# Optimization experiments

Measured on AMD Instinct MI355X. Metric: run time of the kernel, lower is better.

The kernel has to match this reference:

```python
import jax, jax.numpy as jnp
import numpy as np

N = 4_000_000   # total points, 4 per frame
E = N // 4      # edges per subset (idx % 4 == 1, 2, 3)
SQRT2 = float(np.sqrt(2.0))
SQRT3 = float(np.sqrt(3.0))


def _smear(d, num, start=0.0, stop=5.0):
    # GaussianSmearing: exp(-0.5/dx^2 * (d - mu_k)^2), mu_k = linspace(start, stop, num)
    offsets = jnp.linspace(start, stop, num, dtype=d.dtype)
    coeff = -0.5 / (offsets[1] - offsets[0]) ** 2
    return jnp.exp(coeff * (d[:, None] - offsets[None, :]) ** 2)


def setup_inputs() -> dict:
    key = jax.random.key(0)
    ks = jax.random.split(key, 12)
    w = lambda k, s: jax.random.normal(k, s, jnp.float32) * 0.1
    return {
        "ligand_pos": jax.random.normal(ks[0], (N, 3), jnp.float32),
        "receptor_pos": jax.random.normal(ks[1], (N, 3), jnp.float32),
        "W1_sso": w(ks[2], (5, 4, 20)),   # 0e x 0e -> 0e
        "W1_svv": w(ks[3], (5, 5)),       # 0e x 1e -> 1e
        "W1_vsv": w(ks[4], (4, 5)),       # 1e x 0e -> 1e
        "W1_vvo": w(ks[5], (20,)),        # 1e x 1e -> 0e
        "W1_vvv": w(ks[6], (5,)),         # 1e x 1e -> 1e
        "W2_sso": w(ks[7], (20, 5, 9)),
        "W2_svv": w(ks[8], (20,)),
        "W2_vsv": w(ks[9], (5, 5)),
        "W2_vvo": w(ks[10], (5, 9)),
        "W2_vvv": w(ks[11], (5,)),
    }


def reference(ligand_pos, receptor_pos, W1_sso, W1_svv, W1_vsv, W1_vvo, W1_vvv,
              W2_sso, W2_svv, W2_vsv, W2_vvo, W2_vvv):
    edge_vec = ligand_pos - receptor_pos                      # [N,3]
    dist = jnp.sqrt(jnp.sum(edge_vec * edge_vec, -1) + 1e-12)  # [N]
    unit = edge_vec / dist[:, None]

    emb5 = _smear(dist, 5)  # scalars for '5x0e' inputs (features 1, 3)
    emb4 = _smear(dist, 4)  # scalars for '4x0e' input (features 2)

    # edge subsets idx % 4 == 1, 2, 3 (strided gathers)
    s1, v1 = emb5[1::4], unit[1::4]   # [E,5], [E,3]
    s2, v2 = emb4[2::4], unit[2::4]   # [E,4], [E,3]
    s3, v3 = emb5[3::4], unit[3::4]   # [E,5], [E,3]

    # ---- tp1: (5x0e + 1e) x (4x0e + 1e) -> 20x0e + 5x1e ----
    dot12 = jnp.sum(v1 * v2, -1) / SQRT3        # CG 1e x 1e -> 0e
    cross12 = jnp.cross(v1, v2) / SQRT2         # CG 1e x 1e -> 1e
    out_s = (jnp.einsum('ei,ej,ijk->ek', s1, s2, W1_sso)
             + dot12[:, None] * W1_vvo[None, :]) / np.sqrt(21.0)   # fan_in 5*4+1
    out_v = (jnp.einsum('ei,ec,ik->ekc', s1, v2, W1_svv)
             + jnp.einsum('ec,ej,jk->ekc', v1, s2, W1_vsv)
             + cross12[:, None, :] * W1_vvv[None, :, None]) / np.sqrt(10.0)  # fan_in 5+4+1

    # ---- tp2: (20x0e + 5x1e) x (5x0e + 1e) -> 9x0e + 1x1e ----
    dot2 = jnp.einsum('ekc,ec->ek', out_v, v3) / SQRT3          # [E,5]
    cross2 = jnp.cross(out_v, v3[:, None, :]) / SQRT2           # [E,5,3]
    o_s = (jnp.einsum('ei,ej,ijk->ek', out_s, s3, W2_sso)
           + jnp.einsum('ek,ko->eo', dot2, W2_vvo)) / np.sqrt(105.0)  # fan_in 100+5
    o_v = (jnp.einsum('ei,ec,i->ec', out_s, v3, W2_svv)
           + jnp.einsum('ekc,ej,kj->ec', out_v, s3, W2_vsv)
           + jnp.einsum('ekc,k->ec', cross2, W2_vvv)) / np.sqrt(50.0)  # fan_in 20+25+5

    out = jnp.concatenate([o_s, o_v], -1)  # [E,12]
    s_rot, s_tr = out[:, 0:3], out[:, 3:6]
    t_rot, t_tr = out[:, 6:9], out[:, 9:12]
    return jnp.stack([s_rot, s_tr, t_rot, t_tr], 0)  # [4,E,3]
```

## Files before the change

kernel.cpp:

```cpp
#include <hip/hip_runtime.h>
#include <math.h>


#define WS_W12  0
#define WS_WV   900
#define WS_WS   945
#define WS_CS   965
#define WS_SVV  966
#define WS_VSV  991
#define WS_VVV1 1011
#define WS_VSV2 1016
#define WS_VVV2 1041
#define WS_VVO2 1046
#define WS_TOT  1091

__global__ __launch_bounds__(256) void fds_precompose(
    const float* __restrict__ W1_sso, const float* __restrict__ W1_svv,
    const float* __restrict__ W1_vsv, const float* __restrict__ W1_vvo,
    const float* __restrict__ W1_vvv, const float* __restrict__ W2_sso,
    const float* __restrict__ W2_svv, const float* __restrict__ W2_vsv,
    const float* __restrict__ W2_vvo, const float* __restrict__ W2_vvv,
    float* __restrict__ ws)
{
    const float I2 = 0.70710678118654752f, I3 = 0.57735026918962576f;
    const float I10 = 0.31622776601683794f, I21 = 0.21821789023599239f;
    const float I105 = 0.09759000729485332f, I50 = 0.14142135623730950f;
    int tid = threadIdx.x;
    for (int idx = tid; idx < 900; idx += 256) {
        int o = idx % 9, j3 = (idx / 9) % 5, ij = idx / 45;
        float acc = 0.f;
        for (int k2 = 0; k2 < 20; k2++)
            acc = fmaf(W1_sso[ij * 20 + k2], W2_sso[(k2 * 5 + j3) * 9 + o], acc);
        ws[WS_W12 + idx] = acc * (I21 * I105);
    }
    for (int idx = tid; idx < 45; idx += 256) {
        int o = idx % 9, j3 = idx / 9;
        float acc = 0.f;
        for (int k2 = 0; k2 < 20; k2++)
            acc = fmaf(W1_vvo[k2], W2_sso[(k2 * 5 + j3) * 9 + o], acc);
        ws[WS_WV + idx] = acc * (I21 * I105 * I3);
    }
    for (int idx = tid; idx < 20; idx += 256) {
        float acc = 0.f;
        for (int k2 = 0; k2 < 20; k2++)
            acc = fmaf(W1_sso[idx * 20 + k2], W2_svv[k2], acc);
        ws[WS_WS + idx] = acc * (I21 * I50);
    }
    if (tid == 0) {
        float acc = 0.f;
        for (int k2 = 0; k2 < 20; k2++) acc = fmaf(W1_vvo[k2], W2_svv[k2], acc);
        ws[WS_CS] = acc * (I21 * I50 * I3);
    }
    for (int idx = tid; idx < 25; idx += 256) ws[WS_SVV + idx] = W1_svv[idx] * I10;
    for (int idx = tid; idx < 20; idx += 256) ws[WS_VSV + idx] = W1_vsv[idx] * I10;
    for (int idx = tid; idx < 5; idx += 256)  ws[WS_VVV1 + idx] = W1_vvv[idx] * (I10 * I2);
    for (int idx = tid; idx < 25; idx += 256) ws[WS_VSV2 + idx] = W2_vsv[idx] * I50;
    for (int idx = tid; idx < 5; idx += 256)  ws[WS_VVV2 + idx] = W2_vvv[idx] * (I2 * I50);
    for (int idx = tid; idx < 45; idx += 256) ws[WS_VVO2 + idx] = W2_vvo[idx] * (I3 * I105);
}

__global__ __launch_bounds__(256) void fds_kernel(
    const float* __restrict__ lig, const float* __restrict__ rec,
    const float* __restrict__ W12, const float* __restrict__ WV,
    const float* __restrict__ WSp, const float* __restrict__ CSp,
    const float* __restrict__ SVV, const float* __restrict__ VSV,
    const float* __restrict__ VVV1, const float* __restrict__ VSV2,
    const float* __restrict__ VVV2, const float* __restrict__ VVO2,
    float* __restrict__ out, int E)
{
    const float C5 = -0.32f;
    const float C4 = -0.18f;
    const float EK1  = 0.60653065971263342f;
    const float EK4  = 0.13533528323661270f;
    const float EK9  = 0.011108996538242306f;
    const float EK16 = 3.3546262790251185e-4f;
    const float EM1  = 0.36787944117144233f;

    int e = blockIdx.x * blockDim.x + threadIdx.x;
    if (e >= E) return;

    const float4* lp = (const float4*)lig + 3 * (size_t)e;
    const float4* rp = (const float4*)rec + 3 * (size_t)e;
    float4 l0 = lp[0], l1 = lp[1], l2 = lp[2];
    float4 r0 = rp[0], r1 = rp[1], r2 = rp[2];

    float e1x = l0.w - r0.w, e1y = l1.x - r1.x, e1z = l1.y - r1.y;
    float e2x = l1.z - r1.z, e2y = l1.w - r1.w, e2z = l2.x - r2.x;
    float e3x = l2.y - r2.y, e3y = l2.z - r2.z, e3z = l2.w - r2.w;

    float q1 = fmaf(e1x, e1x, fmaf(e1y, e1y, e1z * e1z)) + 1e-12f;
    float q2 = fmaf(e2x, e2x, fmaf(e2y, e2y, e2z * e2z)) + 1e-12f;
    float q3 = fmaf(e3x, e3x, fmaf(e3y, e3y, e3z * e3z)) + 1e-12f;
    float ri1 = rsqrtf(q1), ri2 = rsqrtf(q2), ri3 = rsqrtf(q3);
    float d1 = q1 * ri1, d2 = q2 * ri2, d3 = q3 * ri3;
    float v1x = e1x * ri1, v1y = e1y * ri1, v1z = e1z * ri1;
    float v2x = e2x * ri2, v2y = e2y * ri2, v2z = e2z * ri2;
    float v3x = e3x * ri3, v3y = e3y * ri3, v3z = e3z * ri3;

    float s1[5], s3[5], s2[4];
    float r3;
    {
        float E0 = __expf(C5 * d1 * d1), r = __expf(0.8f * d1);
        float rr = r * r, u = E0 * r, v = E0 * rr;
        s1[0] = E0; s1[1] = u * EK1; s1[2] = v * EK4;
        s1[3] = v * r * EK9; s1[4] = v * rr * EK16;
    }
    {
        float E0 = __expf(C5 * d3 * d3); r3 = __expf(0.8f * d3);
        float rr = r3 * r3, u = E0 * r3, v = E0 * rr;
        s3[0] = E0; s3[1] = u * EK1; s3[2] = v * EK4;
        s3[3] = v * r3 * EK9; s3[4] = v * rr * EK16;
    }
    {
        float E0 = __expf(C4 * d2 * d2), r = __expf(0.6f * d2);
        float rr = r * r;
        s2[0] = E0; s2[1] = E0 * r * EK1; s2[2] = E0 * rr * EK4;
        s2[3] = E0 * rr * r * EK9;
    }

    float dot12 = fmaf(v1x, v2x, fmaf(v1y, v2y, v1z * v2z));
    float cr12x = v1y * v2z - v1z * v2y;
    float cr12y = v1z * v2x - v1x * v2z;
    float cr12z = v1x * v2y - v1y * v2x;

    float A[5], B[5];
#pragma unroll
    for (int k = 0; k < 5; k++) {
        float a = 0.f, b = 0.f;
#pragma unroll
        for (int i = 0; i < 5; i++) a = fmaf(s1[i], SVV[i * 5 + k], a);
#pragma unroll
        for (int j = 0; j < 4; j++) b = fmaf(s2[j], VSV[j * 5 + k], b);
        A[k] = a; B[k] = b;
    }
    float ov[5][3];
#pragma unroll
    for (int k = 0; k < 5; k++) {
        float w = VVV1[k];
        ov[k][0] = fmaf(A[k], v2x, fmaf(B[k], v1x, cr12x * w));
        ov[k][1] = fmaf(A[k], v2y, fmaf(B[k], v1y, cr12y * w));
        ov[k][2] = fmaf(A[k], v2z, fmaf(B[k], v1z, cr12z * w));
    }

    float dot2[5];
#pragma unroll
    for (int k = 0; k < 5; k++)
        dot2[k] = fmaf(ov[k][0], v3x, fmaf(ov[k][1], v3y, ov[k][2] * v3z));

    float accs[9];
#pragma unroll
    for (int o = 0; o < 9; o++) accs[o] = 0.f;
#pragma unroll
    for (int k = 0; k < 5; k++)
#pragma unroll
        for (int o = 0; o < 9; o++) accs[o] = fmaf(dot2[k], VVO2[k * 9 + o], accs[o]);

    float av0 = 0.f, av1 = 0.f, av2 = 0.f;
#pragma unroll
    for (int k = 0; k < 5; k++) {
        float c = 0.f;
#pragma unroll
        for (int j = 0; j < 5; j++) c = fmaf(s3[j], VSV2[k * 5 + j], c);
        float w = VVV2[k];
        float cx = ov[k][1] * v3z - ov[k][2] * v3y;
        float cy = ov[k][2] * v3x - ov[k][0] * v3z;
        float cz = ov[k][0] * v3y - ov[k][1] * v3x;
        av0 = fmaf(ov[k][0], c, fmaf(cx, w, av0));
        av1 = fmaf(ov[k][1], c, fmaf(cy, w, av1));
        av2 = fmaf(ov[k][2], c, fmaf(cz, w, av2));
    }

    float p12[20];
#pragma unroll
    for (int i = 0; i < 5; i++)
#pragma unroll
        for (int j = 0; j < 4; j++) p12[i * 4 + j] = s1[i] * s2[j];

    float S = dot12 * CSp[0];
#pragma unroll
    for (int ij = 0; ij < 20; ij++) S = fmaf(p12[ij], WSp[ij], S);
    av0 = fmaf(S, v3x, av0);
    av1 = fmaf(S, v3y, av1);
    av2 = fmaf(S, v3z, av2);

    {
        const float* wj = W12;
        const float* wv = WV;
        float s3c = s3[0];
        float uu = r3 * EK1;
#pragma clang loop unroll(disable)
        for (int j3 = 0; j3 < 5; ++j3) {
            float fv = dot12 * s3c;
#pragma unroll
            for (int o = 0; o < 9; o++) accs[o] = fmaf(fv, wv[o], accs[o]);
#pragma unroll
            for (int ij = 0; ij < 20; ij++) {
                float f = p12[ij] * s3c;
#pragma unroll
                for (int o = 0; o < 9; o++)
                    accs[o] = fmaf(f, wj[ij * 45 + o], accs[o]);
            }
            s3c *= uu; uu *= EM1;
            wj += 9; wv += 9;
        }
    }

    size_t E3 = (size_t)E * 3;
    size_t b = (size_t)e * 3;
    out[b + 0]          = accs[0];
    out[b + 1]          = accs[1];
    out[b + 2]          = accs[2];
    out[E3 + b + 0]     = accs[3];
    out[E3 + b + 1]     = accs[4];
    out[E3 + b + 2]     = accs[5];
    out[2 * E3 + b + 0] = accs[6];
    out[2 * E3 + b + 1] = accs[7];
    out[2 * E3 + b + 2] = accs[8];
    out[3 * E3 + b + 0] = av0;
    out[3 * E3 + b + 1] = av1;
    out[3 * E3 + b + 2] = av2;
}

extern "C" void kernel_launch(void* const* d_in, const int* in_sizes, int n_in,
                              void* d_out, int out_size, void* d_ws, size_t ws_size,
                              hipStream_t stream) {
    const float* lig    = (const float*)d_in[0];
    const float* rec    = (const float*)d_in[1];
    const float* W1_sso = (const float*)d_in[2];
    const float* W1_svv = (const float*)d_in[3];
    const float* W1_vsv = (const float*)d_in[4];
    const float* W1_vvo = (const float*)d_in[5];
    const float* W1_vvv = (const float*)d_in[6];
    const float* W2_sso = (const float*)d_in[7];
    const float* W2_svv = (const float*)d_in[8];
    const float* W2_vsv = (const float*)d_in[9];
    const float* W2_vvo = (const float*)d_in[10];
    const float* W2_vvv = (const float*)d_in[11];
    float* ws = (float*)d_ws;

    fds_precompose<<<1, 256, 0, stream>>>(W1_sso, W1_svv, W1_vsv, W1_vvo, W1_vvv,
                                          W2_sso, W2_svv, W2_vsv, W2_vvo, W2_vvv, ws);

    int E = in_sizes[0] / 12;
    int blocks = (E + 255) / 256;
    fds_kernel<<<blocks, 256, 0, stream>>>(
        lig, rec,
        ws + WS_W12, ws + WS_WV, ws + WS_WS, ws + WS_CS,
        ws + WS_SVV, ws + WS_VSV, ws + WS_VVV1, ws + WS_VSV2,
        ws + WS_VVV2, ws + WS_VVO2,
        (float*)d_out, E);
}
```

Before: 52.19 us.

## Pack composed TP weights to fp16 pairs and use fdot2 for the contraction

Precomposed W12 and WS weights are now stored as packed half2 pairs, with the layout reordered so each j3 slice is contiguous. The inner 20x9 contraction uses v_dot2 (fdot2) on fp16 products p12*s3 with fp32 accumulation, halving FMA count and weight loads. This lowers precision of the Gaussian-product features and weights to fp16, which risks accuracy loss, especially for small exponentials that may underflow.

```diff
diff --git a/kernel.cpp b/kernel.cpp
--- a/kernel.cpp
+++ b/kernel.cpp
@@ -2,17 +2,19 @@
 #include <math.h>
 
 
-#define WS_W12  0
-#define WS_WV   900
-#define WS_WS   945
-#define WS_CS   965
-#define WS_SVV  966
-#define WS_VSV  991
-#define WS_VVV1 1011
-#define WS_VSV2 1016
-#define WS_VVV2 1041
-#define WS_VVO2 1046
-#define WS_TOT  1091
+typedef _Float16 h2 __attribute__((ext_vector_type(2)));
+
+#define WS_W12H 0
+#define WS_WV   450
+#define WS_WSH  495
+#define WS_CS   505
+#define WS_SVV  506
+#define WS_VSV  531
+#define WS_VVV1 551
+#define WS_VSV2 556
+#define WS_VVV2 581
+#define WS_VVO2 586
+#define WS_TOT  631
 
 __global__ __launch_bounds__(256) void fds_precompose(
     const float* __restrict__ W1_sso, const float* __restrict__ W1_svv,
@@ -26,12 +28,16 @@
     const float I10 = 0.31622776601683794f, I21 = 0.21821789023599239f;
     const float I105 = 0.09759000729485332f, I50 = 0.14142135623730950f;
     int tid = threadIdx.x;
-    for (int idx = tid; idx < 900; idx += 256) {
-        int o = idx % 9, j3 = (idx / 9) % 5, ij = idx / 45;
-        float acc = 0.f;
-        for (int k2 = 0; k2 < 20; k2++)
-            acc = fmaf(W1_sso[ij * 20 + k2], W2_sso[(k2 * 5 + j3) * 9 + o], acc);
-        ws[WS_W12 + idx] = acc * (I21 * I105);
+    for (int idx = tid; idx < 450; idx += 256) {
+        int o = idx % 9, q = (idx / 9) % 10, j3 = idx / 90;
+        float a0 = 0.f, a1 = 0.f;
+        for (int k2 = 0; k2 < 20; k2++) {
+            float w2 = W2_sso[(k2 * 5 + j3) * 9 + o];
+            a0 = fmaf(W1_sso[(2 * q) * 20 + k2], w2, a0);
+            a1 = fmaf(W1_sso[(2 * q + 1) * 20 + k2], w2, a1);
+        }
+        h2 p = { (_Float16)(a0 * (I21 * I105)), (_Float16)(a1 * (I21 * I105)) };
+        ws[WS_W12H + idx] = __builtin_bit_cast(float, p);
     }
     for (int idx = tid; idx < 45; idx += 256) {
         int o = idx % 9, j3 = idx / 9;
@@ -40,11 +46,14 @@
             acc = fmaf(W1_vvo[k2], W2_sso[(k2 * 5 + j3) * 9 + o], acc);
         ws[WS_WV + idx] = acc * (I21 * I105 * I3);
     }
-    for (int idx = tid; idx < 20; idx += 256) {
-        float acc = 0.f;
-        for (int k2 = 0; k2 < 20; k2++)
-            acc = fmaf(W1_sso[idx * 20 + k2], W2_svv[k2], acc);
-        ws[WS_WS + idx] = acc * (I21 * I50);
+    for (int idx = tid; idx < 10; idx += 256) {
+        float a0 = 0.f, a1 = 0.f;
+        for (int k2 = 0; k2 < 20; k2++) {
+            a0 = fmaf(W1_sso[(2 * idx) * 20 + k2], W2_svv[k2], a0);
+            a1 = fmaf(W1_sso[(2 * idx + 1) * 20 + k2], W2_svv[k2], a1);
+        }
+        h2 p = { (_Float16)(a0 * (I21 * I50)), (_Float16)(a1 * (I21 * I50)) };
+        ws[WS_WSH + idx] = __builtin_bit_cast(float, p);
     }
     if (tid == 0) {
         float acc = 0.f;
@@ -61,8 +70,8 @@
 
 __global__ __launch_bounds__(256) void fds_kernel(
     const float* __restrict__ lig, const float* __restrict__ rec,
-    const float* __restrict__ W12, const float* __restrict__ WV,
-    const float* __restrict__ WSp, const float* __restrict__ CSp,
+    const float* __restrict__ W12Hf, const float* __restrict__ WV,
+    const float* __restrict__ WSHf, const float* __restrict__ CSp,
     const float* __restrict__ SVV, const float* __restrict__ VSV,
     const float* __restrict__ VVV1, const float* __restrict__ VSV2,
     const float* __restrict__ VVV2, const float* __restrict__ VVO2,
@@ -76,6 +85,9 @@
     const float EK16 = 3.3546262790251185e-4f;
     const float EM1  = 0.36787944117144233f;
 
+    const h2* __restrict__ W12H = (const h2*)W12Hf;
+    const h2* __restrict__ WSH  = (const h2*)WSHf;
+
     int e = blockIdx.x * blockDim.x + threadIdx.x;
     if (e >= E) return;
 
@@ -170,21 +182,30 @@
         av2 = fmaf(ov[k][2], c, fmaf(cz, w, av2));
     }
 
-    float p12[20];
-#pragma unroll
-    for (int i = 0; i < 5; i++)
-#pragma unroll
-        for (int j = 0; j < 4; j++) p12[i * 4 + j] = s1[i] * s2[j];
+    h2 p12h[10];
+    {
+        h2 s2h[2];
+        s2h[0] = (h2){ (_Float16)s2[0], (_Float16)s2[1] };
+        s2h[1] = (h2){ (_Float16)s2[2], (_Float16)s2[3] };
+#pragma unroll
+        for (int i = 0; i < 5; i++) {
+            _Float16 s1h = (_Float16)s1[i];
+            h2 s1b = (h2){ s1h, s1h };
+            p12h[i * 2 + 0] = s1b * s2h[0];
+            p12h[i * 2 + 1] = s1b * s2h[1];
+        }
+    }
 
     float S = dot12 * CSp[0];
 #pragma unroll
-    for (int ij = 0; ij < 20; ij++) S = fmaf(p12[ij], WSp[ij], S);
+    for (int q = 0; q < 10; q++)
+        S = __builtin_amdgcn_fdot2(p12h[q], WSH[q], S, false);
     av0 = fmaf(S, v3x, av0);
     av1 = fmaf(S, v3y, av1);
     av2 = fmaf(S, v3z, av2);
 
     {
-        const float* wj = W12;
+        const h2* wj = W12H;
         const float* wv = WV;
         float s3c = s3[0];
         float uu = r3 * EK1;
@@ -193,15 +214,17 @@
             float fv = dot12 * s3c;
 #pragma unroll
             for (int o = 0; o < 9; o++) accs[o] = fmaf(fv, wv[o], accs[o]);
-#pragma unroll
-            for (int ij = 0; ij < 20; ij++) {
-                float f = p12[ij] * s3c;
+            _Float16 sh = (_Float16)s3c;
+            h2 shb = (h2){ sh, sh };
+#pragma unroll
+            for (int q = 0; q < 10; q++) {
+                h2 f = p12h[q] * shb;
 #pragma unroll
                 for (int o = 0; o < 9; o++)
-                    accs[o] = fmaf(f, wj[ij * 45 + o], accs[o]);
+                    accs[o] = __builtin_amdgcn_fdot2(f, wj[q * 9 + o], accs[o], false);
             }
             s3c *= uu; uu *= EM1;
-            wj += 9; wv += 9;
+            wj += 90; wv += 9;
         }
     }
 
@@ -245,7 +268,7 @@
     int blocks = (E + 255) / 256;
     fds_kernel<<<blocks, 256, 0, stream>>>(
         lig, rec,
-        ws + WS_W12, ws + WS_WV, ws + WS_WS, ws + WS_CS,
+        ws + WS_W12H, ws + WS_WV, ws + WS_WSH, ws + WS_CS,
         ws + WS_SVV, ws + WS_VSV, ws + WS_VVV1, ws + WS_VSV2,
         ws + WS_VVV2, ws + WS_VVO2,
         (float*)d_out, E);
```

Result: faster. 47.37 us (-9.2%).
